# Performance work log

Hardware: AMD Instinct MI355X
Metric: run time of the kernel (lower is better)

Reference implementation:

```python
import jax, jax.numpy as jnp
import numpy as np

Y_DIM = 100  # number of speakers (one-hot dim)


def _conv1d(x, w, b, stride=2, pad=1):
    # x: [B, Cin, L], w: [Cout, Cin, K] (torch Conv1d layout)
    out = jax.lax.conv_general_dilated(x, w, (stride,), [(pad, pad)],
                                       dimension_numbers=('NCH', 'OIH', 'NCH'))
    return out + b[None, :, None]


def _deconv1d(x, w, b, stride=2, pad=1):
    # w: [Cin, Cout, K] (torch ConvTranspose1d layout)
    k = w.shape[-1]
    wt = jnp.flip(w, -1).transpose(1, 0, 2)  # -> [Cout, Cin, K]
    out = jax.lax.conv_general_dilated(x, wt, (1,), [(k - 1 - pad, k - 1 - pad)],
                                       lhs_dilation=(stride,),
                                       dimension_numbers=('NCH', 'OIH', 'NCH'))
    return out + b[None, :, None]


def _forward(x, enc, codebook, emb_w, emb_b, dec, mu_w, mu_b, spk_idx):
    h = x[:, None, :]                         # [B, 1, 512]
    for w, b in enc:
        h = jax.nn.relu(_conv1d(h, w, b))
    z = h[:, 0, :]                            # [B, 64]
    # 0.5 * ||z - c||^2 for all codes, via expansion (fused cdist)
    d = 0.5 * (jnp.sum(z * z, 1, keepdims=True)
               - 2.0 * z @ codebook.T
               + jnp.sum(codebook * codebook, 1)[None, :])  # [B, K]
    idx = jnp.argmin(d, axis=1)               # first-min tie-break matches strict '<' loop
    code = codebook[idx]                      # [B, 64]
    y = jax.nn.one_hot(spk_idx, Y_DIM, dtype=x.dtype)
    dec_in = jnp.concatenate([code, y], 1) @ emb_w.T + emb_b  # [B, 64]
    h = dec_in[:, None, :]
    for w, b in dec:
        h = jax.nn.relu(_deconv1d(h, w, b))
    out = (h @ mu_w.T + mu_b)[:, 0, :]        # [B, 512]
    return z, code, out


def setup_inputs() -> dict:
    key = jax.random.key(0)
    ks = jax.random.split(key, 20)
    B, L, D, K, Y = 8192, 512, 64, 512, 100
    s = 0.1
    return {
        'x': jax.random.normal(ks[0], (B, L), jnp.float32),
        'enc_w0': jax.random.normal(ks[1], (32, 1, 4), jnp.float32) * s,
        'enc_b0': jnp.zeros((32,), jnp.float32),
        'enc_w1': jax.random.normal(ks[2], (32, 32, 4), jnp.float32) * s,
        'enc_b1': jnp.zeros((32,), jnp.float32),
        'enc_w2': jax.random.normal(ks[3], (1, 32, 4), jnp.float32) * s,
        'enc_b2': jnp.zeros((1,), jnp.float32),
        'codebook': jax.random.normal(ks[4], (K, D), jnp.float32) * s,
        'emb_w': jax.random.normal(ks[5], (D, Y + D), jnp.float32) * s,
        'emb_b': jnp.zeros((D,), jnp.float32),
        'dec_w0': jax.random.normal(ks[6], (1, 32, 4), jnp.float32) * s,
        'dec_b0': jnp.zeros((32,), jnp.float32),
        'dec_w1': jax.random.normal(ks[7], (32, 32, 4), jnp.float32) * s,
        'dec_b1': jnp.zeros((32,), jnp.float32),
        'dec_w2': jax.random.normal(ks[8], (32, 1, 4), jnp.float32) * s,
        'dec_b2': jnp.zeros((1,), jnp.float32),
        'mu_w': jax.random.normal(ks[9], (L, L), jnp.float32) * s,
        'mu_b': jnp.zeros((L,), jnp.float32),
        'spk_idx': jax.random.randint(ks[10], (B,), 0, Y, jnp.int32),
    }


def reference(x, enc_w0, enc_b0, enc_w1, enc_b1, enc_w2, enc_b2, codebook,
              emb_w, emb_b, dec_w0, dec_b0, dec_w1, dec_b1, dec_w2, dec_b2,
              mu_w, mu_b, spk_idx):
    enc = [(enc_w0, enc_b0), (enc_w1, enc_b1), (enc_w2, enc_b2)]
    dec = [(dec_w0, dec_b0), (dec_w1, dec_b1), (dec_w2, dec_b2)]
    return _forward(x, enc, codebook, emb_w, emb_b, dec, mu_w, mu_b, spk_idx)
```

## Files before the change

### kernel.cpp

```cpp
#include <hip/hip_runtime.h>
#include <hip/hip_bf16.h>

__device__ __forceinline__ float bits2f(unsigned int b) {
    union { unsigned int u; float f; } v; v.u = b; return v.f;
}
__device__ __forceinline__ unsigned short f2bf_bits(float f) {
    union { float f; unsigned int u; } v; v.f = f;
    return (unsigned short)((v.u + 0x7fffu + ((v.u >> 16) & 1u)) >> 16);
}
__device__ __forceinline__ unsigned short f2h_bits(_Float16 h) {
    union { _Float16 f; unsigned short u; } v; v.f = h; return v.u;
}

typedef __attribute__((ext_vector_type(8))) short short8;
typedef __attribute__((ext_vector_type(4))) float f32x4;
typedef _Float16 f16x8 __attribute__((ext_vector_type(8)));

#define AS1 __attribute__((address_space(1)))
#define AS3 __attribute__((address_space(3)))

__device__ __align__(16) unsigned short g_muwb[512 * 512];
__device__ __align__(16) unsigned short g_dec1B[4096];
__device__ __align__(16) unsigned short g_dec2B[5120];
__device__ __align__(16) unsigned short g_encBh[4096];
__device__ __align__(16) unsigned short g_encBl[4096];
__device__ float g_cc[512];
__device__ __align__(16) float g_cbT[64 * 512];
__device__ __align__(16) float g_embwT[164 * 64];

__global__ __launch_bounds__(256)
void k_prep(const float* __restrict__ muw, const float* __restrict__ dw1,
            const float* __restrict__ dw2, const float* __restrict__ ew1,
            const float* __restrict__ cb, const float* __restrict__ embw)
{
    int idx = blockIdx.x * 256 + threadIdx.x;
    if (idx < 262144) { g_muwb[idx] = f2bf_bits(muw[idx]); return; }
    int e = idx - 262144;
    if (e < 4096) {
        const int jsel[4] = {1, 3, 2, 0};
        int pt = e >> 10, o = (e >> 5) & 31, i = e & 31;
        g_dec1B[e] = f2bf_bits(dw1[i * 128 + o * 4 + jsel[pt]]);
        return;
    }
    int f = e - 4096;
    if (f < 5120) {
        int j = f / 320, k = f - j * 320;
        int lam = k >> 5, i = k & 31, q = j >> 1;
        float v = 0.f;
        if ((j & 1) == 0) {
            if (lam == q + 1) v = dw2[4 * i + 1];
            else if (lam == q) v = dw2[4 * i + 3];
        } else {
            if (lam == q + 1) v = dw2[4 * i + 2];
            else if (lam == q + 2) v = dw2[4 * i + 0];
        }
        g_dec2B[f] = f2bf_bits(v);
        return;
    }
    int g = f - 5120;
    if (g < 4096) {
        int j = g >> 10, o = (g >> 5) & 31, i = g & 31;
        float w = ew1[o * 128 + i * 4 + j];
        _Float16 wh = (_Float16)w;
        _Float16 wl = (_Float16)((w - (float)wh) * 2048.0f);
        g_encBh[g] = f2h_bits(wh);
        g_encBl[g] = f2h_bits(wl);
        return;
    }
    int h = g - 4096;
    if (h < 512) {
        const float4* cp = (const float4*)(cb + (size_t)h * 64);
        float cc2 = 0.f;
        #pragma unroll
        for (int q = 0; q < 16; ++q) {
            float4 u = cp[q];
            cc2 += u.x * u.x + u.y * u.y + u.z * u.z + u.w * u.w;
        }
        g_cc[h] = cc2;
        return;
    }
    int m = h - 512;
    if (m < 32768) {
        int d = m >> 9, c = m & 511;
        g_cbT[m] = cb[(size_t)c * 64 + d];
        return;
    }
    int n2 = m - 32768;
    if (n2 < 10496) {
        int k = n2 >> 6, j = n2 & 63;
        g_embwT[n2] = embw[(size_t)j * 164 + k];
    }
}

__global__ __launch_bounds__(256, 2)
void k_encoder(const float* __restrict__ x,
               const float* __restrict__ ew0, const float* __restrict__ eb0,
               const float* __restrict__ eb1,
               const float* __restrict__ ew2, const float* __restrict__ eb2,
               float* __restrict__ z_out)
{
    const int tid  = threadIdx.x;
    const int lane = tid & 63;
    const int w    = tid >> 6;
    const int rloc = w >> 1;
    const int wh   = w & 1;
    const int row  = blockIdx.x * 2 + rloc;

    __shared__ __align__(16) float POOL[2 * 4688];
    float* ws = POOL + rloc * 4688;
    float* xs = ws;
    float* h2 = ws + 520;

    const int r = lane & 15, kc = lane >> 4;
    const float biaN0 = eb1[r], biaN1 = eb1[16 + r];

    const float* xrow = x + (size_t)row * 512;
    #pragma unroll
    for (int q = 0; q < 4; ++q) {
        const int ch = wh * 4 + q;
        xs[3 + lane + 64 * ch] = xrow[lane + 64 * ch];
    }
    if (wh == 0) {
        if (lane < 3) xs[lane] = 0.f;
        h2[(lane >> 1) * 130 + 2 + (lane & 1)] = 0.f;
    } else {
        if (lane < 3) xs[515 + lane] = 0.f;
        if (lane < 2) { int gi = 64 + lane; h2[(gi >> 1) * 130 + 2 + (gi & 1)] = 0.f; }
    }

    f16x8 Bh[2][4], Bl[2][4];
    #pragma unroll
    for (int nt = 0; nt < 2; ++nt)
        #pragma unroll
        for (int j = 0; j < 4; ++j) {
            const int off = (j * 32 + nt * 16 + r) * 32 + kc * 8;
            Bh[nt][j] = *(const f16x8*)(g_encBh + off);
            Bl[nt][j] = *(const f16x8*)(g_encBl + off);
        }
    float4 Wv[8]; float b0v[8];
    #pragma unroll
    for (int i = 0; i < 8; ++i) {
        Wv[i]  = *(const float4*)(ew0 + (kc * 8 + i) * 4);
        b0v[i] = eb0[kc * 8 + i];
    }
    __syncthreads();

    #pragma unroll 2
    for (int mi = 0; mi < 4; ++mi) {
        const int m = 4 * wh + mi;
        const int t2 = m * 16 + r;
        float xw[10];
        {
            const float* xwin = xs + 4 * t2;
            #pragma unroll
            for (int q = 0; q < 10; ++q) xw[q] = xwin[q];
        }
        f16x8 ah0, ah1, ah2, ah3, al0, al1, al2, al3;
        #pragma unroll
        for (int i = 0; i < 8; ++i) {
            const float4 W = Wv[i];
            const float b0 = b0v[i];
            float v0 = fmaxf(b0 + xw[0] * W.x + xw[1] * W.y + xw[2] * W.z + xw[3] * W.w, 0.f);
            float v1 = fmaxf(b0 + xw[2] * W.x + xw[3] * W.y + xw[4] * W.z + xw[5] * W.w, 0.f);
            float v2 = fmaxf(b0 + xw[4] * W.x + xw[5] * W.y + xw[6] * W.z + xw[7] * W.w, 0.f);
            float v3 = fmaxf(b0 + xw[6] * W.x + xw[7] * W.y + xw[8] * W.z + xw[9] * W.w, 0.f);
            _Float16 hh0 = (_Float16)v0, hh1 = (_Float16)v1;
            _Float16 hh2 = (_Float16)v2, hh3 = (_Float16)v3;
            _Float16 ll0 = (_Float16)((v0 - (float)hh0) * 2048.0f);
            _Float16 ll1 = (_Float16)((v1 - (float)hh1) * 2048.0f);
            _Float16 ll2 = (_Float16)((v2 - (float)hh2) * 2048.0f);
            _Float16 ll3 = (_Float16)((v3 - (float)hh3) * 2048.0f);
            ah0[i] = hh0; al0[i] = ll0;
            ah1[i] = hh1; al1[i] = ll1;
            ah2[i] = hh2; al2[i] = ll2;
            ah3[i] = hh3; al3[i] = ll3;
        }
        {
            const f16x8 Z8 = {(_Float16)0.f, (_Float16)0.f, (_Float16)0.f, (_Float16)0.f,
                              (_Float16)0.f, (_Float16)0.f, (_Float16)0.f, (_Float16)0.f};
            if (t2 == 0)   { ah0 = Z8; al0 = Z8; }
            if (t2 == 127) { ah3 = Z8; al3 = Z8; }
        }
        const int t0 = m * 16;
        #pragma unroll
        for (int nt = 0; nt < 2; ++nt) {
            f32x4 ahh = (f32x4){0.f, 0.f, 0.f, 0.f};
            f32x4 am  = (f32x4){0.f, 0.f, 0.f, 0.f};
            f32x4 all_= (f32x4){0.f, 0.f, 0.f, 0.f};
            ahh = __builtin_amdgcn_mfma_f32_16x16x32_f16(ah0, Bh[nt][0], ahh, 0, 0, 0);
            am  = __builtin_amdgcn_mfma_f32_16x16x32_f16(ah0, Bl[nt][0], am,  0, 0, 0);
            am  = __builtin_amdgcn_mfma_f32_16x16x32_f16(al0, Bh[nt][0], am,  0, 0, 0);
            all_= __builtin_amdgcn_mfma_f32_16x16x32_f16(al0, Bl[nt][0], all_,0, 0, 0);
            ahh = __builtin_amdgcn_mfma_f32_16x16x32_f16(ah1, Bh[nt][1], ahh, 0, 0, 0);
            am  = __builtin_amdgcn_mfma_f32_16x16x32_f16(ah1, Bl[nt][1], am,  0, 0, 0);
            am  = __builtin_amdgcn_mfma_f32_16x16x32_f16(al1, Bh[nt][1], am,  0, 0, 0);
            all_= __builtin_amdgcn_mfma_f32_16x16x32_f16(al1, Bl[nt][1], all_,0, 0, 0);
            ahh = __builtin_amdgcn_mfma_f32_16x16x32_f16(ah2, Bh[nt][2], ahh, 0, 0, 0);
            am  = __builtin_amdgcn_mfma_f32_16x16x32_f16(ah2, Bl[nt][2], am,  0, 0, 0);
            am  = __builtin_amdgcn_mfma_f32_16x16x32_f16(al2, Bh[nt][2], am,  0, 0, 0);
            all_= __builtin_amdgcn_mfma_f32_16x16x32_f16(al2, Bl[nt][2], all_,0, 0, 0);
            ahh = __builtin_amdgcn_mfma_f32_16x16x32_f16(ah3, Bh[nt][3], ahh, 0, 0, 0);
            am  = __builtin_amdgcn_mfma_f32_16x16x32_f16(ah3, Bl[nt][3], am,  0, 0, 0);
            am  = __builtin_amdgcn_mfma_f32_16x16x32_f16(al3, Bh[nt][3], am,  0, 0, 0);
            all_= __builtin_amdgcn_mfma_f32_16x16x32_f16(al3, Bl[nt][3], all_,0, 0, 0);
            const float bia = nt ? biaN1 : biaN0;
            float* orow = h2 + (nt * 16 + r) * 130 + 4 + t0 + kc * 4;
            #pragma unroll
            for (int e = 0; e < 4; ++e)
                orow[e] = fmaxf(ahh[e] + 4.8828125e-4f * am[e]
                                + 2.384185791015625e-07f * all_[e] + bia, 0.f);
        }
    }
    __syncthreads();

    if (wh == 0) {
        const int t = lane;
        float pg[4];
        #pragma unroll
        for (int gg = 0; gg < 4; ++gg) {
            float p = 0.f;
            #pragma unroll
            for (int ii = 0; ii < 8; ++ii) {
                const int i = gg * 8 + ii;
                const float4 W = *(const float4*)(ew2 + i * 4);
                const float* hr = h2 + i * 130 + 4;
                p += hr[2 * t - 1] * W.x + hr[2 * t] * W.y
                   + hr[2 * t + 1] * W.z + hr[2 * t + 2] * W.w;
            }
            pg[gg] = p;
        }
        float zv = fmaxf(pg[0] + pg[1] + pg[2] + pg[3] + eb2[0], 0.f);
        z_out[(size_t)row * 64 + t] = zv;
    }
}

__global__ __launch_bounds__(256)
void k_enc_tail(const float* __restrict__ z_in, const float* __restrict__ cb,
                const float* __restrict__ embb,
                const int* __restrict__ spk,
                float* __restrict__ code_out, float* __restrict__ din_g)
{
    const int blk  = blockIdx.x;
    const int tid  = threadIdx.x;
    const int lane = tid & 63;
    const int wv   = tid >> 6;

    __shared__ __align__(16) float zs[8][64];
    __shared__ __align__(16) float csf[8][64];
    __shared__ float zzv[8];
    __shared__ float redv[4][8];
    __shared__ int   redi[4][8];
    __shared__ int   sidxs[8];

    const int jq = tid & 63;
    const int rq = tid >> 6;

    #pragma unroll
    for (int ch = 0; ch < 2; ++ch) {
        const int rr = rq + ch * 4;
        zs[rr][jq] = z_in[((size_t)blk * 8 + rr) * 64 + jq];
    }
    __syncthreads();

    if (tid < 8) {
        float4 zr[16];
        #pragma unroll
        for (int q = 0; q < 16; ++q) zr[q] = *(const float4*)(&zs[tid][4 * q]);
        float u[32];
        #pragma unroll
        for (int q = 0; q < 8; ++q) {
            u[4 * q + 0] = __fadd_rn(__fmul_rn(zr[q].x, zr[q].x), __fmul_rn(zr[q + 8].x, zr[q + 8].x));
            u[4 * q + 1] = __fadd_rn(__fmul_rn(zr[q].y, zr[q].y), __fmul_rn(zr[q + 8].y, zr[q + 8].y));
            u[4 * q + 2] = __fadd_rn(__fmul_rn(zr[q].z, zr[q].z), __fmul_rn(zr[q + 8].z, zr[q + 8].z));
            u[4 * q + 3] = __fadd_rn(__fmul_rn(zr[q].w, zr[q].w), __fmul_rn(zr[q + 8].w, zr[q + 8].w));
        }
        #pragma unroll
        for (int off = 16; off; off >>= 1)
            #pragma unroll
            for (int i = 0; i < off; ++i) u[i] = __fadd_rn(u[i], u[i + off]);
        zzv[tid] = u[0];
    }

    float acc[8][2];
    #pragma unroll
    for (int r2 = 0; r2 < 8; ++r2) { acc[r2][0] = 0.f; acc[r2][1] = 0.f; }

    #pragma unroll 4
    for (int dq = 0; dq < 16; ++dq) {
        float4 zv[8];
        #pragma unroll
        for (int r2 = 0; r2 < 8; ++r2) zv[r2] = *(const float4*)(&zs[r2][4 * dq]);
        #pragma unroll
        for (int dd = 0; dd < 4; ++dd) {
            const int d = 4 * dq + dd;
            const float w0 = g_cbT[d * 512 + tid];
            const float w1 = g_cbT[d * 512 + 256 + tid];
            #pragma unroll
            for (int r2 = 0; r2 < 8; ++r2) {
                const float zd = (dd == 0) ? zv[r2].x : (dd == 1) ? zv[r2].y
                               : (dd == 2) ? zv[r2].z : zv[r2].w;
                acc[r2][0] = fmaf(w0, zd, acc[r2][0]);
                acc[r2][1] = fmaf(w1, zd, acc[r2][1]);
            }
        }
    }
    __syncthreads();

    {
        const float cc0 = g_cc[tid], cc1 = g_cc[tid + 256];
        float best[8]; int bidx[8];
        #pragma unroll
        for (int r2 = 0; r2 < 8; ++r2) {
            const float zz = zzv[r2];
            float d0 = 0.5f * (zz - 2.f * acc[r2][0] + cc0);
            float d1 = 0.5f * (zz - 2.f * acc[r2][1] + cc1);
            best[r2] = d0; bidx[r2] = tid;
            if (d1 < best[r2]) { best[r2] = d1; bidx[r2] = tid + 256; }
        }
        #pragma unroll
        for (int off = 32; off; off >>= 1) {
            #pragma unroll
            for (int r2 = 0; r2 < 8; ++r2) {
                float od = __shfl_down(best[r2], off);
                int   oi = __shfl_down(bidx[r2], off);
                if (od < best[r2] || (od == best[r2] && oi < bidx[r2])) {
                    best[r2] = od; bidx[r2] = oi;
                }
            }
        }
        if (lane == 0) {
            #pragma unroll
            for (int r2 = 0; r2 < 8; ++r2) { redv[wv][r2] = best[r2]; redi[wv][r2] = bidx[r2]; }
        }
    }
    __syncthreads();
    if (tid < 8) {
        float bd = redv[0][tid]; int bi = redi[0][tid];
        #pragma unroll
        for (int w = 1; w < 4; ++w)
            if (redv[w][tid] < bd || (redv[w][tid] == bd && redi[w][tid] < bi)) {
                bd = redv[w][tid]; bi = redi[w][tid];
            }
        sidxs[tid] = min(max(bi, 0), 511);
    }
    __syncthreads();

    #pragma unroll
    for (int ch = 0; ch < 2; ++ch) {
        const int rr = rq + ch * 4;
        const int sx = sidxs[rr];
        const float cv = cb[(size_t)sx * 64 + jq];
        code_out[((size_t)blk * 8 + rr) * 64 + jq] = cv;
        csf[rr][jq] = cv;
    }
    __syncthreads();
    #pragma unroll
    for (int ch = 0; ch < 2; ++ch) {
        const int rr = rq + ch * 4;
        const size_t b2 = (size_t)blk * 8 + rr;
        float pg[4];
        #pragma unroll
        for (int gg = 0; gg < 4; ++gg) {
            float p = 0.f;
            #pragma unroll
            for (int q = 0; q < 4; ++q) {
                const int k0 = 16 * gg + 4 * q;
                const float w0 = g_embwT[(k0 + 0) * 64 + jq];
                const float w1 = g_embwT[(k0 + 1) * 64 + jq];
                const float w2 = g_embwT[(k0 + 2) * 64 + jq];
                const float w3 = g_embwT[(k0 + 3) * 64 + jq];
                p += w0 * csf[rr][k0 + 0] + w1 * csf[rr][k0 + 1]
                   + w2 * csf[rr][k0 + 2] + w3 * csf[rr][k0 + 3];
            }
            pg[gg] = p;
        }
        float a = pg[0] + pg[1] + pg[2] + pg[3]
                + embb[jq] + g_embwT[(64 + spk[b2]) * 64 + jq];
        din_g[b2 * 64 + jq] = a;
    }
}

__global__ __launch_bounds__(256)
void k_decoder(const float* __restrict__ din_g,
               const float* __restrict__ dw0, const float* __restrict__ db0,
               const float* __restrict__ db1, const float* __restrict__ db2,
               unsigned short* __restrict__ hdec)
{
    const int gidx = blockIdx.x;
    const int bblk = gidx >> 3;
    const int m0   = (gidx & 7) * 16;
    const int tid  = threadIdx.x;
    const int lane = tid & 63;
    const int q    = tid >> 6;

    __shared__ __align__(16) float        dins[16 * 68];
    __shared__ __align__(16) unsigned int d2c[4][10 * 16 * 18];

    {
        int b = tid >> 4, j4 = tid & 15;
        float4 v = *(const float4*)(din_g + ((size_t)bblk * 16 + b) * 64 + j4 * 4);
        float* dr = dins + b * 68 + 1 + j4 * 4;
        dr[0] = v.x; dr[1] = v.y; dr[2] = v.z; dr[3] = v.w;
        if (j4 == 0) { dins[b * 68] = 0.f; dins[b * 68 + 65] = 0.f; }
    }

    const int r = lane & 15, kc = lane >> 4;
    const float bia2 = db2[0];

    float4 Wa[4], Wb[4]; float ba0v[4], ba1v[4];
    #pragma unroll
    for (int j = 0; j < 4; ++j) {
        const int pp = 4 * kc + j;
        Wa[j] = *(const float4*)(dw0 + 8 * pp);
        Wb[j] = *(const float4*)(dw0 + 8 * pp + 4);
        ba0v[j] = db0[2 * pp];
        ba1v[j] = db0[2 * pp + 1];
    }
    short8 B00[2], B10[2], B01[2], B11[2];
    #pragma unroll
    for (int p = 0; p < 2; ++p) {
        const unsigned short* Bp = g_dec1B + p * 2048;
        B00[p] = *(const short8*)(Bp + (r) * 32 + kc * 8);
        B10[p] = *(const short8*)(Bp + 1024 + (r) * 32 + kc * 8);
        B01[p] = *(const short8*)(Bp + (16 + r) * 32 + kc * 8);
        B11[p] = *(const short8*)(Bp + 1024 + (16 + r) * 32 + kc * 8);
    }
    const float bv0 = db1[r], bv1 = db1[16 + r];
    __syncthreads();

    unsigned int d1r[6][4];
    const float* dn = dins + r * 68 + 1;
    #pragma unroll
    for (int tl = 0; tl < 6; ++tl) {
        const int s = m0 - 1 + 4 * q + tl;
        const bool inb = (s >= 0 && s < 128);
        const int m = s >> 1;
        #pragma unroll
        for (int j = 0; j < 4; ++j) {
            unsigned int pk = 0u;
            if (inb) {
                float v0, v1;
                if (s & 1) { v0 = ba0v[j] + dn[m] * Wa[j].z + dn[m + 1] * Wa[j].x;
                             v1 = ba1v[j] + dn[m] * Wb[j].z + dn[m + 1] * Wb[j].x; }
                else       { v0 = ba0v[j] + dn[m] * Wa[j].y + dn[m - 1] * Wa[j].w;
                             v1 = ba1v[j] + dn[m] * Wb[j].y + dn[m - 1] * Wb[j].w; }
                pk = (unsigned int)f2bf_bits(fmaxf(v0, 0.f))
                   | ((unsigned int)f2bf_bits(fmaxf(v1, 0.f)) << 16);
            }
            d1r[tl][j] = pk;
        }
    }

    unsigned short* d2u = (unsigned short*)(d2c[q]);
    const int tb = 2 * m0 - 1 + 8 * q;
    #pragma unroll
    for (int sgl = 0; sgl < 10; ++sgl) {
        const int p     = 1 - (sgl & 1);
        const int tauAl = (sgl + 1) >> 1;
        const int tauBl = p ? tauAl + 1 : tauAl - 1;
        const int t = tb + sgl;
        if (t >= 0 && t < 256) {
            union { unsigned int u[4]; short8 s8; } am_, ap_;
            am_.u[0] = d1r[tauAl][0]; am_.u[1] = d1r[tauAl][1];
            am_.u[2] = d1r[tauAl][2]; am_.u[3] = d1r[tauAl][3];
            ap_.u[0] = d1r[tauBl][0]; ap_.u[1] = d1r[tauBl][1];
            ap_.u[2] = d1r[tauBl][2]; ap_.u[3] = d1r[tauBl][3];
            f32x4 acc0 = (f32x4){0.f, 0.f, 0.f, 0.f};
            f32x4 acc1 = (f32x4){0.f, 0.f, 0.f, 0.f};
            acc0 = __builtin_amdgcn_mfma_f32_16x16x32_bf16(am_.s8, B00[p], acc0, 0, 0, 0);
            acc0 = __builtin_amdgcn_mfma_f32_16x16x32_bf16(ap_.s8, B10[p], acc0, 0, 0, 0);
            acc1 = __builtin_amdgcn_mfma_f32_16x16x32_bf16(am_.s8, B01[p], acc1, 0, 0, 0);
            acc1 = __builtin_amdgcn_mfma_f32_16x16x32_bf16(ap_.s8, B11[p], acc1, 0, 0, 0);
            #pragma unroll
            for (int e = 0; e < 4; ++e) {
                int bC = kc * 4 + e;
                d2u[sgl * 576 + bC * 36 + r]      = f2bf_bits(fmaxf(acc0[e] + bv0, 0.f));
                d2u[sgl * 576 + bC * 36 + 16 + r] = f2bf_bits(fmaxf(acc1[e] + bv1, 0.f));
            }
        } else {
            #pragma unroll
            for (int e = 0; e < 4; ++e) {
                int bC = kc * 4 + e;
                d2u[sgl * 576 + bC * 36 + r]      = 0;
                d2u[sgl * 576 + bC * 36 + 16 + r] = 0;
            }
        }
    }

    {
        f32x4 acc = (f32x4){0.f, 0.f, 0.f, 0.f};
        #pragma unroll
        for (int kap = 0; kap < 10; ++kap) {
            short8 A = *(const short8*)(d2u + kap * 576 + r * 36 + kc * 8);
            short8 B = *(const short8*)(g_dec2B + r * 320 + kap * 32 + kc * 8);
            acc = __builtin_amdgcn_mfma_f32_16x16x32_bf16(A, B, acc, 0, 0, 0);
        }
        const int n = 4 * m0 + 16 * q + r;
        #pragma unroll
        for (int e = 0; e < 4; ++e) {
            int b = kc * 4 + e;
            hdec[((size_t)bblk * 16 + b) * 512 + n] = f2bf_bits(fmaxf(acc[e] + bia2, 0.f));
        }
    }
}

__global__ __launch_bounds__(256)
void k_mu_gemm(const unsigned short* __restrict__ A,
               const float* __restrict__ bias,
               float* __restrict__ C)
{
    __shared__ unsigned short As[128 * 32];
    __shared__ unsigned short Bs[128 * 32];
    const int tid  = threadIdx.x;
    const int lane = tid & 63;
    const int wid  = tid >> 6;
    const int bm   = blockIdx.x & 63;
    const int bn   = blockIdx.x >> 6;
    const int wm   = (wid & 1) * 64;
    const int wn   = (wid >> 1) * 64;
    const unsigned short* Ab = A + (size_t)bm * 128 * 512;
    const unsigned short* Bb = g_muwb + (size_t)bn * 128 * 512;

    f32x4 acc[4][4];
    #pragma unroll
    for (int i = 0; i < 4; ++i)
        #pragma unroll
        for (int j = 0; j < 4; ++j)
            acc[i][j] = (f32x4){0.f, 0.f, 0.f, 0.f};

    const int r  = lane & 15;
    const int kc = lane >> 4;

    for (int ks = 0; ks < 16; ++ks) {
        const int k0 = ks * 32;
        #pragma unroll
        for (int q = 0; q < 2; ++q) {
            const int off  = q * 4096 + tid * 16;
            const int row  = off >> 6;
            const int colb = off & 63;
            const char* ga = (const char*)Ab + (size_t)row * 1024 + (size_t)k0 * 2 + colb;
            const char* gb = (const char*)Bb + (size_t)row * 1024 + (size_t)k0 * 2 + colb;
            char* la = (char*)As + q * 4096 + wid * 1024;
            char* lb = (char*)Bs + q * 4096 + wid * 1024;
            __builtin_amdgcn_global_load_lds((AS1 const unsigned int*)ga, (AS3 unsigned int*)la, 16, 0, 0);
            __builtin_amdgcn_global_load_lds((AS1 const unsigned int*)gb, (AS3 unsigned int*)lb, 16, 0, 0);
        }
        __syncthreads();

        short8 af[4], bf[4];
        #pragma unroll
        for (int mf = 0; mf < 4; ++mf)
            af[mf] = *(const short8*)&As[(wm + mf * 16 + r) * 32 + kc * 8];
        #pragma unroll
        for (int nf = 0; nf < 4; ++nf)
            bf[nf] = *(const short8*)&Bs[(wn + nf * 16 + r) * 32 + kc * 8];
        #pragma unroll
        for (int mf = 0; mf < 4; ++mf)
            #pragma unroll
            for (int nf = 0; nf < 4; ++nf)
                acc[mf][nf] = __builtin_amdgcn_mfma_f32_16x16x32_bf16(af[mf], bf[nf], acc[mf][nf], 0, 0, 0);
        __syncthreads();
    }

    const int col = lane & 15;
    const int rg  = lane >> 4;
    float bv[4];
    #pragma unroll
    for (int nf = 0; nf < 4; ++nf)
        bv[nf] = bias[bn * 128 + wn + nf * 16 + col];
    #pragma unroll
    for (int mf = 0; mf < 4; ++mf)
        #pragma unroll
        for (int nf = 0; nf < 4; ++nf)
            #pragma unroll
            for (int e = 0; e < 4; ++e) {
                int m = bm * 128 + wm + mf * 16 + rg * 4 + e;
                int n = bn * 128 + wn + nf * 16 + col;
                C[(size_t)m * 512 + n] = acc[mf][nf][e] + bv[nf];
            }
}

extern "C" void kernel_launch(void* const* d_in, const int* in_sizes, int n_in,
                              void* d_out, int out_size, void* d_ws, size_t ws_size,
                              hipStream_t stream) {
    const float* x    = (const float*)d_in[0];
    const float* ew0  = (const float*)d_in[1];
    const float* eb0  = (const float*)d_in[2];
    const float* ew1  = (const float*)d_in[3];
    const float* eb1  = (const float*)d_in[4];
    const float* ew2  = (const float*)d_in[5];
    const float* eb2  = (const float*)d_in[6];
    const float* cb   = (const float*)d_in[7];
    const float* embw = (const float*)d_in[8];
    const float* embb = (const float*)d_in[9];
    const float* dw0  = (const float*)d_in[10];
    const float* db0  = (const float*)d_in[11];
    const float* dw1  = (const float*)d_in[12];
    const float* db1  = (const float*)d_in[13];
    const float* dw2  = (const float*)d_in[14];
    const float* db2  = (const float*)d_in[15];
    const float* muw  = (const float*)d_in[16];
    const float* mub  = (const float*)d_in[17];
    const int*   spk  = (const int*)d_in[18];

    float* zout = (float*)d_out;
    float* cout = zout + (size_t)8192 * 64;
    float* yout = zout + (size_t)2 * 8192 * 64;
    float* din_g = zout + (size_t)8192 * 576;

    unsigned short* hdec = (unsigned short*)d_ws;

    k_prep<<<dim3(1247), dim3(256), 0, stream>>>(muw, dw1, dw2, ew1, cb, embw);

    k_encoder<<<dim3(4096), dim3(256), 0, stream>>>(
        x, ew0, eb0, eb1, ew2, eb2, zout);

    k_enc_tail<<<dim3(1024), dim3(256), 0, stream>>>(
        zout, cb, embb, spk, cout, din_g);

    k_decoder<<<dim3(4096), dim3(256), 0, stream>>>(din_g, dw0, db0, db1, db2, hdec);

    k_mu_gemm<<<dim3(256), dim3(256), 0, stream>>>(hdec, mub, yout);
}
```

Baseline: 159.3 us.

## Reuse encoder conv0 taps via lane shuffles and shrink mu GEMM M-tile

In the encoder, the four A-fragments of conv0 output overlap between consecutive 16-row m-tiles. The new code computes only the two new fragments per tile and derives the other two from the previous tile with cross-lane shuffles, roughly halving the conv0 VALU work and fp16 split conversions. Separately, the mu GEMM tile drops from 128x128 to 64x128, doubling the block count to 512 for better CU occupancy, at the cost of re-reading the B tile more often.

```diff
diff --git a/kernel.cpp b/kernel.cpp
--- a/kernel.cpp
+++ b/kernel.cpp
@@ -15,6 +15,20 @@
 typedef __attribute__((ext_vector_type(8))) short short8;
 typedef __attribute__((ext_vector_type(4))) float f32x4;
 typedef _Float16 f16x8 __attribute__((ext_vector_type(8)));
+
+__device__ __forceinline__ f16x8 shuf_prev16(f16x8 cur, f16x8 carry, int lane) {
+    union U { f16x8 h; int u[4]; } a, c, o;
+    a.h = cur; c.h = carry;
+    const int src15 = (lane & 48) | 15;
+    const bool isr0 = (lane & 15) == 0;
+    #pragma unroll
+    for (int k = 0; k < 4; ++k) {
+        int up  = __shfl_up(a.u[k], 1, 16);
+        int c15 = __shfl(c.u[k], src15, 64);
+        o.u[k] = isr0 ? c15 : up;
+    }
+    return o.h;
+}
 
 #define AS1 __attribute__((address_space(1)))
 #define AS3 __attribute__((address_space(3)))
@@ -113,6 +127,8 @@
 
     const int r = lane & 15, kc = lane >> 4;
     const float biaN0 = eb1[r], biaN1 = eb1[16 + r];
+    const f16x8 Z8 = {(_Float16)0.f, (_Float16)0.f, (_Float16)0.f, (_Float16)0.f,
+                      (_Float16)0.f, (_Float16)0.f, (_Float16)0.f, (_Float16)0.f};
 
     const float* xrow = x + (size_t)row * 512;
     #pragma unroll
@@ -145,9 +161,10 @@
     }
     __syncthreads();
 
-    #pragma unroll 2
-    for (int mi = 0; mi < 4; ++mi) {
-        const int m = 4 * wh + mi;
+    f16x8 c2h, c2l, c3h, c3l;
+
+    {
+        const int m = 4 * wh;
         const int t2 = m * 16 + r;
         float xw[10];
         {
@@ -175,12 +192,8 @@
             ah2[i] = hh2; al2[i] = ll2;
             ah3[i] = hh3; al3[i] = ll3;
         }
-        {
-            const f16x8 Z8 = {(_Float16)0.f, (_Float16)0.f, (_Float16)0.f, (_Float16)0.f,
-                              (_Float16)0.f, (_Float16)0.f, (_Float16)0.f, (_Float16)0.f};
-            if (t2 == 0)   { ah0 = Z8; al0 = Z8; }
-            if (t2 == 127) { ah3 = Z8; al3 = Z8; }
-        }
+        if (t2 == 0) { ah0 = Z8; al0 = Z8; }
+        c2h = ah2; c2l = al2; c3h = ah3; c3l = al3;
         const int t0 = m * 16;
         #pragma unroll
         for (int nt = 0; nt < 2; ++nt) {
@@ -211,6 +224,63 @@
                                 + 2.384185791015625e-07f * all_[e] + bia, 0.f);
         }
     }
+
+    #pragma unroll
+    for (int mi = 1; mi < 4; ++mi) {
+        const int m = 4 * wh + mi;
+        const int t2 = m * 16 + r;
+        const float* xwin = xs + 4 * t2;
+        const float x4 = xwin[4], x5 = xwin[5], x6 = xwin[6];
+        const float x7 = xwin[7], x8 = xwin[8], x9 = xwin[9];
+        f16x8 ah2, ah3, al2, al3;
+        #pragma unroll
+        for (int i = 0; i < 8; ++i) {
+            const float4 W = Wv[i];
+            const float b0 = b0v[i];
+            float v2 = fmaxf(b0 + x4 * W.x + x5 * W.y + x6 * W.z + x7 * W.w, 0.f);
+            float v3 = fmaxf(b0 + x6 * W.x + x7 * W.y + x8 * W.z + x9 * W.w, 0.f);
+            _Float16 hh2 = (_Float16)v2, hh3 = (_Float16)v3;
+            _Float16 ll2 = (_Float16)((v2 - (float)hh2) * 2048.0f);
+            _Float16 ll3 = (_Float16)((v3 - (float)hh3) * 2048.0f);
+            ah2[i] = hh2; al2[i] = ll2;
+            ah3[i] = hh3; al3[i] = ll3;
+        }
+        f16x8 ah0 = shuf_prev16(ah2, c2h, lane);
+        f16x8 al0 = shuf_prev16(al2, c2l, lane);
+        f16x8 ah1 = shuf_prev16(ah3, c3h, lane);
+        f16x8 al1 = shuf_prev16(al3, c3l, lane);
+        c2h = ah2; c2l = al2; c3h = ah3; c3l = al3;
+        if (t2 == 127) { ah3 = Z8; al3 = Z8; }
+        const int t0 = m * 16;
+        #pragma unroll
+        for (int nt = 0; nt < 2; ++nt) {
+            f32x4 ahh = (f32x4){0.f, 0.f, 0.f, 0.f};
+            f32x4 am  = (f32x4){0.f, 0.f, 0.f, 0.f};
+            f32x4 all_= (f32x4){0.f, 0.f, 0.f, 0.f};
+            ahh = __builtin_amdgcn_mfma_f32_16x16x32_f16(ah0, Bh[nt][0], ahh, 0, 0, 0);
+            am  = __builtin_amdgcn_mfma_f32_16x16x32_f16(ah0, Bl[nt][0], am,  0, 0, 0);
+            am  = __builtin_amdgcn_mfma_f32_16x16x32_f16(al0, Bh[nt][0], am,  0, 0, 0);
+            all_= __builtin_amdgcn_mfma_f32_16x16x32_f16(al0, Bl[nt][0], all_,0, 0, 0);
+            ahh = __builtin_amdgcn_mfma_f32_16x16x32_f16(ah1, Bh[nt][1], ahh, 0, 0, 0);
+            am  = __builtin_amdgcn_mfma_f32_16x16x32_f16(ah1, Bl[nt][1], am,  0, 0, 0);
+            am  = __builtin_amdgcn_mfma_f32_16x16x32_f16(al1, Bh[nt][1], am,  0, 0, 0);
+            all_= __builtin_amdgcn_mfma_f32_16x16x32_f16(al1, Bl[nt][1], all_,0, 0, 0);
+            ahh = __builtin_amdgcn_mfma_f32_16x16x32_f16(ah2, Bh[nt][2], ahh, 0, 0, 0);
+            am  = __builtin_amdgcn_mfma_f32_16x16x32_f16(ah2, Bl[nt][2], am,  0, 0, 0);
+            am  = __builtin_amdgcn_mfma_f32_16x16x32_f16(al2, Bh[nt][2], am,  0, 0, 0);
+            all_= __builtin_amdgcn_mfma_f32_16x16x32_f16(al2, Bl[nt][2], all_,0, 0, 0);
+            ahh = __builtin_amdgcn_mfma_f32_16x16x32_f16(ah3, Bh[nt][3], ahh, 0, 0, 0);
+            am  = __builtin_amdgcn_mfma_f32_16x16x32_f16(ah3, Bl[nt][3], am,  0, 0, 0);
+            am  = __builtin_amdgcn_mfma_f32_16x16x32_f16(al3, Bh[nt][3], am,  0, 0, 0);
+            all_= __builtin_amdgcn_mfma_f32_16x16x32_f16(al3, Bl[nt][3], all_,0, 0, 0);
+            const float bia = nt ? biaN1 : biaN0;
+            float* orow = h2 + (nt * 16 + r) * 130 + 4 + t0 + kc * 4;
+            #pragma unroll
+            for (int e = 0; e < 4; ++e)
+                orow[e] = fmaxf(ahh[e] + 4.8828125e-4f * am[e]
+                                + 2.384185791015625e-07f * all_[e] + bia, 0.f);
+        }
+    }
     __syncthreads();
 
     if (wh == 0) {
@@ -509,21 +579,21 @@
                const float* __restrict__ bias,
                float* __restrict__ C)
 {
-    __shared__ unsigned short As[128 * 32];
+    __shared__ unsigned short As[64 * 32];
     __shared__ unsigned short Bs[128 * 32];
     const int tid  = threadIdx.x;
     const int lane = tid & 63;
     const int wid  = tid >> 6;
-    const int bm   = blockIdx.x & 63;
-    const int bn   = blockIdx.x >> 6;
-    const int wm   = (wid & 1) * 64;
+    const int bm   = blockIdx.x & 127;
+    const int bn   = blockIdx.x >> 7;
+    const int wm   = (wid & 1) * 32;
     const int wn   = (wid >> 1) * 64;
-    const unsigned short* Ab = A + (size_t)bm * 128 * 512;
+    const unsigned short* Ab = A + (size_t)bm * 64 * 512;
     const unsigned short* Bb = g_muwb + (size_t)bn * 128 * 512;
 
-    f32x4 acc[4][4];
-    #pragma unroll
-    for (int i = 0; i < 4; ++i)
+    f32x4 acc[2][4];
+    #pragma unroll
+    for (int i = 0; i < 2; ++i)
         #pragma unroll
         for (int j = 0; j < 4; ++j)
             acc[i][j] = (f32x4){0.f, 0.f, 0.f, 0.f};
@@ -533,29 +603,34 @@
 
     for (int ks = 0; ks < 16; ++ks) {
         const int k0 = ks * 32;
+        {
+            const int off  = tid * 16;
+            const int row  = off >> 6;
+            const int colb = off & 63;
+            const char* ga = (const char*)Ab + (size_t)row * 1024 + (size_t)k0 * 2 + colb;
+            char* la = (char*)As + wid * 1024;
+            __builtin_amdgcn_global_load_lds((AS1 const unsigned int*)ga, (AS3 unsigned int*)la, 16, 0, 0);
+        }
         #pragma unroll
         for (int q = 0; q < 2; ++q) {
             const int off  = q * 4096 + tid * 16;
             const int row  = off >> 6;
             const int colb = off & 63;
-            const char* ga = (const char*)Ab + (size_t)row * 1024 + (size_t)k0 * 2 + colb;
             const char* gb = (const char*)Bb + (size_t)row * 1024 + (size_t)k0 * 2 + colb;
-            char* la = (char*)As + q * 4096 + wid * 1024;
             char* lb = (char*)Bs + q * 4096 + wid * 1024;
-            __builtin_amdgcn_global_load_lds((AS1 const unsigned int*)ga, (AS3 unsigned int*)la, 16, 0, 0);
             __builtin_amdgcn_global_load_lds((AS1 const unsigned int*)gb, (AS3 unsigned int*)lb, 16, 0, 0);
         }
         __syncthreads();
 
-        short8 af[4], bf[4];
-        #pragma unroll
-        for (int mf = 0; mf < 4; ++mf)
+        short8 af[2], bf[4];
+        #pragma unroll
+        for (int mf = 0; mf < 2; ++mf)
             af[mf] = *(const short8*)&As[(wm + mf * 16 + r) * 32 + kc * 8];
         #pragma unroll
         for (int nf = 0; nf < 4; ++nf)
             bf[nf] = *(const short8*)&Bs[(wn + nf * 16 + r) * 32 + kc * 8];
         #pragma unroll
-        for (int mf = 0; mf < 4; ++mf)
+        for (int mf = 0; mf < 2; ++mf)
             #pragma unroll
             for (int nf = 0; nf < 4; ++nf)
                 acc[mf][nf] = __builtin_amdgcn_mfma_f32_16x16x32_bf16(af[mf], bf[nf], acc[mf][nf], 0, 0, 0);
@@ -569,12 +644,12 @@
     for (int nf = 0; nf < 4; ++nf)
         bv[nf] = bias[bn * 128 + wn + nf * 16 + col];
     #pragma unroll
-    for (int mf = 0; mf < 4; ++mf)
+    for (int mf = 0; mf < 2; ++mf)
         #pragma unroll
         for (int nf = 0; nf < 4; ++nf)
             #pragma unroll
             for (int e = 0; e < 4; ++e) {
-                int m = bm * 128 + wm + mf * 16 + rg * 4 + e;
+                int m = bm * 64 + wm + mf * 16 + rg * 4 + e;
                 int n = bn * 128 + wn + nf * 16 + col;
                 C[(size_t)m * 512 + n] = acc[mf][nf][e] + bv[nf];
             }
@@ -620,5 +695,5 @@
 
     k_decoder<<<dim3(4096), dim3(256), 0, stream>>>(din_g, dw0, db0, db1, db2, hdec);
 
-    k_mu_gemm<<<dim3(256), dim3(256), 0, stream>>>(hdec, mub, yout);
-}
+    k_mu_gemm<<<dim3(512), dim3(256), 0, stream>>>(hdec, mub, yout);
+}
```

Measured after the change: 164.2 us. 3.1% more time.
